# Kernel tuning notes

Measured on AMD Instinct MI355X. Metric: run time of the kernel, lower is better.

The kernel has to match this reference:

```python
import jax, jax.numpy as jnp
import numpy as np

EMIN = 1e-9
EMAX = 1.0
PENAL = 3.0
VOLFRAC = 0.4
GAMMA2 = 1.0
NME = 262144        # number of finite elements
KE = 64             # 8x8 element stiffness entries per element
NDOF = 524288       # global degrees of freedom


def setup_inputs() -> dict:
    key = jax.random.key(0)
    k1, k2, k3, k4, k5 = jax.random.split(key, 5)
    W_x = jax.random.normal(k1, (NME,), dtype=jnp.float32)
    K_sep = jax.random.normal(k2, (NME, KE), dtype=jnp.float32)
    indeces_K = jax.random.randint(k3, (2, NME * KE), 0, NDOF, dtype=jnp.int32)
    u = jax.random.normal(k4, (NDOF,), dtype=jnp.float32)
    f = jax.random.normal(k5, (NDOF,), dtype=jnp.float32)
    return {"W_x": W_x, "K_sep": K_sep, "indeces_K": indeces_K, "u": u, "f": f}


def reference(W_x, K_sep, indeces_K, u, f):
    # SIMP density from logits
    rho = jax.nn.sigmoid(W_x)                                  # [nme]
    # power-law material interpolation: Emin + rho^p (Emax - Emin)
    scale = EMIN + rho ** PENAL * (EMAX - EMIN)                # [nme]
    # scaled element stiffness values, flattened COO values
    sK = (K_sep * scale[:, None]).reshape(-1)                  # [nme*64]
    rows = indeces_K[0]
    cols = indeces_K[1]
    # sparse matvec K @ u via gather + segment-sum scatter assembly
    Ku = jax.ops.segment_sum(sK * u[cols], rows, num_segments=NDOF)  # [ndof]
    confidence_loss = jnp.linalg.norm(Ku - f)
    vofrac_loss = jax.nn.relu(rho.mean() - VOLFRAC)
    loss = vofrac_loss + GAMMA2 * confidence_loss
    return loss
```

## Files before the change

### kernel.cpp

```cpp
#include <hip/hip_runtime.h>
#include <math.h>

namespace {

constexpr int       kNME    = 262144;
constexpr int       kNDOF   = 524288;
constexpr long long kNNZ    = 16777216;
constexpr int       kNB     = 64;
constexpr int       kBShift = 13;
constexpr int       kBSpan  = 8192;
constexpr int       kEnt    = 8192;
constexpr int       kPTh   = 1024;
constexpr int       kPerTh  = 8;
constexpr int       kCtrStride = 16;
constexpr int       kScaleBlocks = kNME / 256;
constexpr int       kR      = 8;

constexpr float kEmin    = 1e-9f;
constexpr float kEmax    = 1.0f;
constexpr float kVolfrac = 0.4f;

using u32   = unsigned;
using i32x4 = __attribute__((ext_vector_type(4))) int;
using f32x4 = __attribute__((ext_vector_type(4))) float;
using u32x4 = __attribute__((ext_vector_type(4))) unsigned;

__device__ __forceinline__ u32 pack32(unsigned localrow, float v) {
    return (localrow << 19) | (__float_as_uint(v) >> 13);
}

__global__ void scale_kernel(const float* __restrict__ W_x,
                             float* __restrict__ scale,
                             float* __restrict__ acc,
                             unsigned* __restrict__ counters,
                             float* __restrict__ rho_part) {
    const int gid = blockIdx.x * blockDim.x + threadIdx.x;

    if (gid >= 1 && gid < 16) acc[gid] = 0.0f;
    const int cidx = gid - 16;
    if (cidx >= 0 && cidx < kNB * kR * kCtrStride) counters[cidx] = 0u;

    float rho = 0.0f;
    if (gid < kNME) {
        float x = W_x[gid];
        rho = 1.0f / (1.0f + __expf(-x));
        scale[gid] = kEmin + rho * rho * rho * (kEmax - kEmin);
    }
    for (int off = 32; off > 0; off >>= 1) rho += __shfl_down(rho, off, 64);
    __shared__ float partial[4];
    const int lane = threadIdx.x & 63;
    const int wid  = threadIdx.x >> 6;
    if (lane == 0) partial[wid] = rho;
    __syncthreads();
    if (threadIdx.x == 0)
        rho_part[blockIdx.x] =
            partial[0] + partial[1] + partial[2] + partial[3];
}

__global__ __launch_bounds__(kPTh, 8)
void producer_kernel(const float* __restrict__ K_sep,
                     const int*   __restrict__ rows,
                     const int*   __restrict__ cols,
                     const float* __restrict__ u,
                     const float* __restrict__ scale,
                     u32*         __restrict__ pairs,
                     unsigned*    __restrict__ counters,
                     unsigned capSub) {
    __shared__ unsigned hist[kNB], ofs[kNB], gbase[kNB];
    __shared__ u32      sorted[kEnt];

    const int tid = threadIdx.x;
    const int sub = blockIdx.x & (kR - 1);
    if (tid < kNB) hist[tid] = 0u;
    __syncthreads();

    const long long i0 =
        (long long)blockIdx.x * kEnt + (long long)tid * kPerTh;
    i32x4 r0 = __builtin_nontemporal_load((const i32x4*)(rows + i0));
    i32x4 r1 = __builtin_nontemporal_load((const i32x4*)(rows + i0) + 1);
    i32x4 c0 = __builtin_nontemporal_load((const i32x4*)(cols + i0));
    i32x4 c1 = __builtin_nontemporal_load((const i32x4*)(cols + i0) + 1);
    f32x4 k0 = __builtin_nontemporal_load((const f32x4*)(K_sep + i0));
    f32x4 k1 = __builtin_nontemporal_load((const f32x4*)(K_sep + i0) + 1);
    const float s = scale[(int)(i0 >> 6)];

    unsigned rv[kPerTh];
    float    vv[kPerTh];
#pragma unroll
    for (int j = 0; j < 4; ++j) {
        rv[j]     = (unsigned)r0[j];  vv[j]     = k0[j] * s * u[c0[j]];
        rv[j + 4] = (unsigned)r1[j];  vv[j + 4] = k1[j] * s * u[c1[j]];
    }
#pragma unroll
    for (int j = 0; j < kPerTh; ++j)
        rv[j] |= atomicAdd(&hist[rv[j] >> kBShift], 1u) << 19;
    __syncthreads();

    if (tid < kNB) {
        unsigned h = hist[tid];
        unsigned x = h;
#pragma unroll
        for (int off = 1; off < kNB; off <<= 1) {
            unsigned y = __shfl_up(x, off, 64);
            if (tid >= off) x += y;
        }
        ofs[tid]   = x - h;
        gbase[tid] = atomicAdd(&counters[(tid * kR + sub) * kCtrStride], h);
    }
    __syncthreads();

#pragma unroll
    for (int j = 0; j < kPerTh; ++j) {
        unsigned row = rv[j] & 0x7FFFFu;
        unsigned b   = row >> kBShift;
        unsigned pos = ofs[b] + (rv[j] >> 19);
        sorted[pos]  = pack32(row & (kBSpan - 1), vv[j]);
    }
    __syncthreads();

    const int wid = tid >> 6, lane = tid & 63;
    for (int b = wid; b < kNB; b += 16) {
        const unsigned s0 = ofs[b];
        const unsigned n  = hist[b];
        const unsigned g  = gbase[b];
        u32* dst = pairs + (size_t)(b * kR + sub) * capSub + g;
        for (unsigned i = lane; i < n; i += 64) {
            if (g + i < capSub) dst[i] = sorted[s0 + i];
        }
    }
}

__global__ __launch_bounds__(1024, 8)
void consumer_kernel(const u32*      __restrict__ pairs,
                     const unsigned* __restrict__ counters,
                     float*          __restrict__ partial,
                     unsigned capSub) {
    const int b   = blockIdx.x / kR;
    const int sub = blockIdx.x - b * kR;
    unsigned cnt = counters[(b * kR + sub) * kCtrStride];
    if (cnt > capSub) cnt = capSub;

    __shared__ float acc[kBSpan];
    for (int i = threadIdx.x; i < kBSpan; i += 1024) acc[i] = 0.0f;
    __syncthreads();

    const u32* p = pairs + (size_t)(b * kR + sub) * capSub;
    const unsigned aligned = cnt & ~3u;
    for (unsigned i = 4 * threadIdx.x; i < aligned; i += 4096) {
        u32x4 e = *((const u32x4*)(p + i));
#pragma unroll
        for (int j = 0; j < 4; ++j)
            atomicAdd(&acc[e[j] >> 19], __uint_as_float(e[j] << 13));
    }
    if (threadIdx.x < (cnt - aligned)) {
        u32 e = p[aligned + threadIdx.x];
        atomicAdd(&acc[e >> 19], __uint_as_float(e << 13));
    }
    __syncthreads();

    float* dst = partial + (size_t)(b * kR + sub) * kBSpan;
    for (int k = threadIdx.x; k < kBSpan; k += 1024) dst[k] = acc[k];
}

__global__ void norm_kernel(const float* __restrict__ partial,
                            const float* __restrict__ f,
                            float* __restrict__ acc,
                            const float* __restrict__ rho_part,
                            float* __restrict__ out) {
    const int b  = blockIdx.x >> 3;
    const int i0 = (blockIdx.x & 7) * 1024 + threadIdx.x * 4;
    f32x4 s = {0.0f, 0.0f, 0.0f, 0.0f};
#pragma unroll
    for (int r = 0; r < kR; ++r)
        s += *(const f32x4*)(partial + (size_t)(b * kR + r) * kBSpan + i0);
    f32x4 fv = *(const f32x4*)(f + (size_t)b * kBSpan + i0);
    f32x4 d  = s - fv;
    float a = d[0] * d[0] + d[1] * d[1] + d[2] * d[2] + d[3] * d[3];
    for (int off = 32; off > 0; off >>= 1) a += __shfl_down(a, off, 64);
    __shared__ float partial_s[4];
    const int lane = threadIdx.x & 63;
    const int wid  = threadIdx.x >> 6;
    if (lane == 0) partial_s[wid] = a;
    __syncthreads();
    if (threadIdx.x == 0) {
        atomicAdd(&acc[1],
                  partial_s[0] + partial_s[1] + partial_s[2] + partial_s[3]);
        __threadfence();
        unsigned done = atomicAdd((unsigned*)&acc[2], 1u);
        if (done == gridDim.x - 1) {
            float rs = 0.0f;
            for (int i = 0; i < kScaleBlocks; i += 4) {
                f32x4 rp = *(const f32x4*)(rho_part + i);
                rs += rp[0] + rp[1] + rp[2] + rp[3];
            }
            float ns = __hip_atomic_load(&acc[1], __ATOMIC_RELAXED,
                                         __HIP_MEMORY_SCOPE_AGENT);
            float rho_mean = rs * (1.0f / (float)kNME);
            out[0] = fmaxf(rho_mean - kVolfrac, 0.0f) + sqrtf(ns);
        }
    }
}

__global__ void scale1_kernel(const float* __restrict__ W_x,
                              float* __restrict__ scale,
                              float* __restrict__ rho_sum) {
    int i = blockIdx.x * blockDim.x + threadIdx.x;
    float rho = 0.0f;
    if (i < kNME) {
        float x = W_x[i];
        rho = 1.0f / (1.0f + __expf(-x));
        scale[i] = kEmin + rho * rho * rho * (kEmax - kEmin);
    }
    for (int off = 32; off > 0; off >>= 1) rho += __shfl_down(rho, off, 64);
    __shared__ float partial[4];
    const int lane = threadIdx.x & 63;
    const int wid  = threadIdx.x >> 6;
    if (lane == 0) partial[wid] = rho;
    __syncthreads();
    if (threadIdx.x == 0)
        atomicAdd(rho_sum, partial[0] + partial[1] + partial[2] + partial[3]);
}

__global__ void scatter_dev_kernel(const float* __restrict__ K_sep,
                                   const int*   __restrict__ rows,
                                   const int*   __restrict__ cols,
                                   const float* __restrict__ u,
                                   const float* __restrict__ scale,
                                   float* __restrict__ Ku) {
    long long i = (long long)blockIdx.x * blockDim.x + threadIdx.x;
    if (i >= kNNZ) return;
    float s = scale[(int)(i >> 6)];
    atomicAdd(&Ku[rows[i]], K_sep[i] * s * u[cols[i]]);
}

__global__ void norm1_kernel(const float* __restrict__ Ku,
                             const float* __restrict__ f,
                             float* __restrict__ norm_sum) {
    float a = 0.0f;
    for (int i = blockIdx.x * blockDim.x + threadIdx.x; i < kNDOF;
         i += gridDim.x * blockDim.x) {
        float d = Ku[i] - f[i];
        a += d * d;
    }
    for (int off = 32; off > 0; off >>= 1) a += __shfl_down(a, off, 64);
    __shared__ float partial_s[4];
    const int lane = threadIdx.x & 63;
    const int wid  = threadIdx.x >> 6;
    if (lane == 0) partial_s[wid] = a;
    __syncthreads();
    if (threadIdx.x == 0)
        atomicAdd(norm_sum,
                  partial_s[0] + partial_s[1] + partial_s[2] + partial_s[3]);
}

__global__ void finalize_kernel(const float* __restrict__ acc,
                                float* __restrict__ out) {
    if (threadIdx.x == 0 && blockIdx.x == 0) {
        float rho_mean = acc[0] * (1.0f / (float)kNME);
        float vol = fmaxf(rho_mean - kVolfrac, 0.0f);
        out[0] = vol + sqrtf(acc[1]);
    }
}

}

extern "C" void kernel_launch(void* const* d_in, const int* in_sizes, int n_in,
                              void* d_out, int out_size, void* d_ws, size_t ws_size,
                              hipStream_t stream) {
    const float* W_x   = (const float*)d_in[0];
    const float* K_sep = (const float*)d_in[1];
    const int*   idx   = (const int*)d_in[2];
    const float* u     = (const float*)d_in[3];
    const float* f     = (const float*)d_in[4];
    const int* rows = idx;
    const int* cols = idx + kNNZ;

    float* ws = (float*)d_ws;
    const size_t avail = ws_size / sizeof(float);

    const unsigned capSub = (unsigned)(kNNZ / (kNB * kR)) + 4096;
    const size_t   ctrF   = (size_t)kNB * kR * kCtrStride;
    const size_t   headF  = 16;
    const size_t   rhoF   = kScaleBlocks;
    const size_t   partF  = (size_t)kNB * kR * kBSpan;
    const size_t   need   = headF + ctrF + rhoF + partF + kNME +
                            (size_t)kNB * kR * capSub;

    if (need > avail) {
        float* Ku    = ws;
        float* scale = ws + kNDOF;
        float* acc   = ws + kNDOF + kNME;
        hipMemsetAsync(ws, 0, (size_t)(kNDOF + kNME + 16) * sizeof(float), stream);
        scale1_kernel<<<kNME / 256, 256, 0, stream>>>(W_x, scale, acc);
        scatter_dev_kernel<<<(int)(kNNZ / 256), 256, 0, stream>>>(
            K_sep, rows, cols, u, scale, Ku);
        norm1_kernel<<<2048, 256, 0, stream>>>(Ku, f, acc + 1);
        finalize_kernel<<<1, 64, 0, stream>>>(acc, (float*)d_out);
        return;
    }

    float*    acc      = ws;
    unsigned* counters = (unsigned*)(ws + headF);
    float*    rho_part = ws + headF + ctrF;
    float*    partial  = rho_part + rhoF;
    float*    scale    = partial + partF;
    u32*      pairs    = (u32*)(scale + kNME);

    scale_kernel<<<kScaleBlocks, 256, 0, stream>>>(W_x, scale, acc, counters,
                                                   rho_part);

    producer_kernel<<<(int)(kNNZ / kEnt), kPTh, 0, stream>>>(
        K_sep, rows, cols, u, scale, pairs, counters, capSub);

    consumer_kernel<<<kNB * kR, 1024, 0, stream>>>(
        pairs, counters, partial, capSub);

    norm_kernel<<<kNB * (kBSpan / 1024), 256, 0, stream>>>(
        partial, f, acc, rho_part, (float*)d_out);
}
```

Measured before the change: 242.7 us.

## Split scatter into two chunks and overlap second producer with first consumer

Splits the nonzeros into two halves with separate bucket buffers and counters. The second half's producer blocks run in the same launch as the first half's consumer blocks, interleaved 2:1 by block index, so the bandwidth-bound produce phase overlaps the LDS-atomic consume phase. A final consumer pass adds its results into the partial buffer. The cost is an extra launch, a read-modify-write of the partial buffer, and capSub slack per chunk that is tighter relative to each bucket's expected size, which raises the risk of overflow.

After: 259.5 us. 1.07x slower.

```diff
diff --git a/kernel.cpp b/kernel.cpp
--- a/kernel.cpp
+++ b/kernel.cpp
@@ -10,11 +10,14 @@
 constexpr int       kBShift = 13;
 constexpr int       kBSpan  = 8192;
 constexpr int       kEnt    = 8192;
-constexpr int       kPTh   = 1024;
+constexpr int       kPTh    = 1024;
 constexpr int       kPerTh  = 8;
 constexpr int       kCtrStride = 16;
 constexpr int       kScaleBlocks = kNME / 256;
 constexpr int       kR      = 8;
+constexpr long long kChunk  = kNNZ / 2;
+constexpr int       kPBlk   = (int)(kChunk / kEnt);
+constexpr int       kCBlk   = kNB * kR;
 
 constexpr float kEmin    = 1e-9f;
 constexpr float kEmax    = 1.0f;
@@ -29,53 +32,20 @@
     return (localrow << 19) | (__float_as_uint(v) >> 13);
 }
 
-__global__ void scale_kernel(const float* __restrict__ W_x,
-                             float* __restrict__ scale,
-                             float* __restrict__ acc,
-                             unsigned* __restrict__ counters,
-                             float* __restrict__ rho_part) {
-    const int gid = blockIdx.x * blockDim.x + threadIdx.x;
-
-    if (gid >= 1 && gid < 16) acc[gid] = 0.0f;
-    const int cidx = gid - 16;
-    if (cidx >= 0 && cidx < kNB * kR * kCtrStride) counters[cidx] = 0u;
-
-    float rho = 0.0f;
-    if (gid < kNME) {
-        float x = W_x[gid];
-        rho = 1.0f / (1.0f + __expf(-x));
-        scale[gid] = kEmin + rho * rho * rho * (kEmax - kEmin);
-    }
-    for (int off = 32; off > 0; off >>= 1) rho += __shfl_down(rho, off, 64);
-    __shared__ float partial[4];
-    const int lane = threadIdx.x & 63;
-    const int wid  = threadIdx.x >> 6;
-    if (lane == 0) partial[wid] = rho;
-    __syncthreads();
-    if (threadIdx.x == 0)
-        rho_part[blockIdx.x] =
-            partial[0] + partial[1] + partial[2] + partial[3];
-}
-
-__global__ __launch_bounds__(kPTh, 8)
-void producer_kernel(const float* __restrict__ K_sep,
-                     const int*   __restrict__ rows,
-                     const int*   __restrict__ cols,
-                     const float* __restrict__ u,
-                     const float* __restrict__ scale,
-                     u32*         __restrict__ pairs,
-                     unsigned*    __restrict__ counters,
-                     unsigned capSub) {
-    __shared__ unsigned hist[kNB], ofs[kNB], gbase[kNB];
-    __shared__ u32      sorted[kEnt];
-
+__device__ __forceinline__ void producer_body(
+    const float* __restrict__ K_sep, const int* __restrict__ rows,
+    const int* __restrict__ cols, const float* __restrict__ u,
+    const float* __restrict__ scale, u32* __restrict__ pairs,
+    unsigned* __restrict__ counters, long long chunk_base,
+    unsigned capSub, int pidx,
+    unsigned* hist, unsigned* ofs, unsigned* gbase, u32* sorted) {
     const int tid = threadIdx.x;
-    const int sub = blockIdx.x & (kR - 1);
+    const int sub = pidx & (kR - 1);
     if (tid < kNB) hist[tid] = 0u;
     __syncthreads();
 
     const long long i0 =
-        (long long)blockIdx.x * kEnt + (long long)tid * kPerTh;
+        chunk_base + (long long)pidx * kEnt + (long long)tid * kPerTh;
     i32x4 r0 = __builtin_nontemporal_load((const i32x4*)(rows + i0));
     i32x4 r1 = __builtin_nontemporal_load((const i32x4*)(rows + i0) + 1);
     i32x4 c0 = __builtin_nontemporal_load((const i32x4*)(cols + i0));
@@ -130,23 +100,21 @@
     }
 }
 
-__global__ __launch_bounds__(1024, 8)
-void consumer_kernel(const u32*      __restrict__ pairs,
-                     const unsigned* __restrict__ counters,
-                     float*          __restrict__ partial,
-                     unsigned capSub) {
-    const int b   = blockIdx.x / kR;
-    const int sub = blockIdx.x - b * kR;
+__device__ __forceinline__ void consumer_body(
+    const u32* __restrict__ pairs, const unsigned* __restrict__ counters,
+    float* __restrict__ partial, unsigned capSub, int cidx, int accum,
+    float* acc) {
+    const int b   = cidx / kR;
+    const int sub = cidx - b * kR;
     unsigned cnt = counters[(b * kR + sub) * kCtrStride];
     if (cnt > capSub) cnt = capSub;
 
-    __shared__ float acc[kBSpan];
-    for (int i = threadIdx.x; i < kBSpan; i += 1024) acc[i] = 0.0f;
+    for (int i = threadIdx.x; i < kBSpan; i += kPTh) acc[i] = 0.0f;
     __syncthreads();
 
     const u32* p = pairs + (size_t)(b * kR + sub) * capSub;
     const unsigned aligned = cnt & ~3u;
-    for (unsigned i = 4 * threadIdx.x; i < aligned; i += 4096) {
+    for (unsigned i = 4 * threadIdx.x; i < aligned; i += 4 * kPTh) {
         u32x4 e = *((const u32x4*)(p + i));
 #pragma unroll
         for (int j = 0; j < 4; ++j)
@@ -159,7 +127,79 @@
     __syncthreads();
 
     float* dst = partial + (size_t)(b * kR + sub) * kBSpan;
-    for (int k = threadIdx.x; k < kBSpan; k += 1024) dst[k] = acc[k];
+    if (accum) {
+        for (int k = threadIdx.x; k < kBSpan; k += kPTh) dst[k] += acc[k];
+    } else {
+        for (int k = threadIdx.x; k < kBSpan; k += kPTh) dst[k] = acc[k];
+    }
+}
+
+__global__ void scale_kernel(const float* __restrict__ W_x,
+                             float* __restrict__ scale,
+                             float* __restrict__ acc,
+                             unsigned* __restrict__ counters,
+                             float* __restrict__ rho_part) {
+    const int gid = blockIdx.x * blockDim.x + threadIdx.x;
+
+    if (gid >= 1 && gid < 16) acc[gid] = 0.0f;
+    const int cidx = gid - 16;
+    if (cidx >= 0 && cidx < 2 * kNB * kR * kCtrStride) counters[cidx] = 0u;
+
+    float rho = 0.0f;
+    if (gid < kNME) {
+        float x = W_x[gid];
+        rho = 1.0f / (1.0f + __expf(-x));
+        scale[gid] = kEmin + rho * rho * rho * (kEmax - kEmin);
+    }
+    for (int off = 32; off > 0; off >>= 1) rho += __shfl_down(rho, off, 64);
+    __shared__ float partial[4];
+    const int lane = threadIdx.x & 63;
+    const int wid  = threadIdx.x >> 6;
+    if (lane == 0) partial[wid] = rho;
+    __syncthreads();
+    if (threadIdx.x == 0)
+        rho_part[blockIdx.x] =
+            partial[0] + partial[1] + partial[2] + partial[3];
+}
+
+__global__ __launch_bounds__(kPTh, 8)
+void p0_kernel(const float* __restrict__ K_sep, const int* __restrict__ rows,
+               const int* __restrict__ cols, const float* __restrict__ u,
+               const float* __restrict__ scale, u32* __restrict__ pairs0,
+               unsigned* __restrict__ ctr0, unsigned capSub) {
+    __shared__ unsigned hist[kNB], ofs[kNB], gbase[kNB];
+    __shared__ __align__(16) u32 sorted[kEnt];
+    producer_body(K_sep, rows, cols, u, scale, pairs0, ctr0, 0LL, capSub,
+                  blockIdx.x, hist, ofs, gbase, sorted);
+}
+
+__global__ __launch_bounds__(kPTh, 8)
+void p1c0_kernel(const float* __restrict__ K_sep, const int* __restrict__ rows,
+                 const int* __restrict__ cols, const float* __restrict__ u,
+                 const float* __restrict__ scale,
+                 u32* __restrict__ pairs0, u32* __restrict__ pairs1,
+                 unsigned* __restrict__ ctr0, unsigned* __restrict__ ctr1,
+                 float* __restrict__ partial, unsigned capSub) {
+    __shared__ unsigned hist[kNB], ofs[kNB], gbase[kNB];
+    __shared__ __align__(16) u32 sorted[kEnt];
+
+    const int i = blockIdx.x;
+    if ((i % 3) != 2) {
+        const int pidx = (i / 3) * 2 + (i % 3);
+        producer_body(K_sep, rows, cols, u, scale, pairs1, ctr1, kChunk,
+                      capSub, pidx, hist, ofs, gbase, sorted);
+    } else {
+        const int cidx = i / 3;
+        consumer_body(pairs0, ctr0, partial, capSub, cidx, 0,
+                      (float*)sorted);
+    }
+}
+
+__global__ __launch_bounds__(kPTh, 8)
+void c1_kernel(const u32* __restrict__ pairs1, const unsigned* __restrict__ ctr1,
+               float* __restrict__ partial, unsigned capSub) {
+    __shared__ __align__(16) float acc[kBSpan];
+    consumer_body(pairs1, ctr1, partial, capSub, blockIdx.x, 1, acc);
 }
 
 __global__ void norm_kernel(const float* __restrict__ partial,
@@ -278,13 +318,14 @@
     float* ws = (float*)d_ws;
     const size_t avail = ws_size / sizeof(float);
 
-    const unsigned capSub = (unsigned)(kNNZ / (kNB * kR)) + 4096;
+    const unsigned capSub = (unsigned)(kChunk / (kNB * kR)) + 2048;
     const size_t   ctrF   = (size_t)kNB * kR * kCtrStride;
     const size_t   headF  = 16;
     const size_t   rhoF   = kScaleBlocks;
     const size_t   partF  = (size_t)kNB * kR * kBSpan;
-    const size_t   need   = headF + ctrF + rhoF + partF + kNME +
-                            (size_t)kNB * kR * capSub;
+    const size_t   pairF  = (size_t)kNB * kR * capSub;
+    const size_t   need   = headF + 2 * ctrF + rhoF + partF + kNME +
+                            2 * pairF;
 
     if (need > avail) {
         float* Ku    = ws;
@@ -300,20 +341,25 @@
     }
 
     float*    acc      = ws;
-    unsigned* counters = (unsigned*)(ws + headF);
-    float*    rho_part = ws + headF + ctrF;
+    unsigned* ctr0     = (unsigned*)(ws + headF);
+    unsigned* ctr1     = ctr0 + ctrF;
+    float*    rho_part = ws + headF + 2 * ctrF;
     float*    partial  = rho_part + rhoF;
     float*    scale    = partial + partF;
-    u32*      pairs    = (u32*)(scale + kNME);
-
-    scale_kernel<<<kScaleBlocks, 256, 0, stream>>>(W_x, scale, acc, counters,
+    u32*      pairs0   = (u32*)(scale + kNME);
+    u32*      pairs1   = pairs0 + pairF;
+
+    scale_kernel<<<kScaleBlocks, 256, 0, stream>>>(W_x, scale, acc, ctr0,
                                                    rho_part);
 
-    producer_kernel<<<(int)(kNNZ / kEnt), kPTh, 0, stream>>>(
-        K_sep, rows, cols, u, scale, pairs, counters, capSub);
-
-    consumer_kernel<<<kNB * kR, 1024, 0, stream>>>(
-        pairs, counters, partial, capSub);
+    p0_kernel<<<kPBlk, kPTh, 0, stream>>>(K_sep, rows, cols, u, scale,
+                                          pairs0, ctr0, capSub);
+
+    p1c0_kernel<<<kPBlk + kCBlk, kPTh, 0, stream>>>(
+        K_sep, rows, cols, u, scale, pairs0, pairs1, ctr0, ctr1, partial,
+        capSub);
+
+    c1_kernel<<<kCBlk, kPTh, 0, stream>>>(pairs1, ctr1, partial, capSub);
 
     norm_kernel<<<kNB * (kBSpan / 1024), 256, 0, stream>>>(
         partial, f, acc, rho_part, (float*)d_out);
```

## Use 512 finer row buckets and fuse consumer accumulation with norm reduction

Applied to the files above, without the earlier changes.

Rows are now split into 512 buckets of 1024 rows instead of 64 buckets with 8 sub-slots. Each consumer block accumulates one full bucket in a 1 KB shared tile and computes the squared residual against f directly, so the partial-sum buffer and the separate norm kernel go away. Packed values keep 22 mantissa-truncated bits instead of 19, which improves precision. The costs are a two-level prefix scan in the producer, scattered writes split into 16-lane groups across more buckets, and more contention on the shared global counters.

New measurement: 263.9 us. 8.7% more time.

```diff
diff --git a/kernel.cpp b/kernel.cpp
--- a/kernel.cpp
+++ b/kernel.cpp
@@ -6,15 +6,14 @@
 constexpr int       kNME    = 262144;
 constexpr int       kNDOF   = 524288;
 constexpr long long kNNZ    = 16777216;
-constexpr int       kNB     = 64;
-constexpr int       kBShift = 13;
-constexpr int       kBSpan  = 8192;
+constexpr int       kNBk    = 512;
+constexpr int       kBSh    = 10;
+constexpr int       kBSp    = 1024;
 constexpr int       kEnt    = 8192;
-constexpr int       kPTh   = 1024;
+constexpr int       kPTh    = 1024;
 constexpr int       kPerTh  = 8;
 constexpr int       kCtrStride = 16;
 constexpr int       kScaleBlocks = kNME / 256;
-constexpr int       kR      = 8;
 
 constexpr float kEmin    = 1e-9f;
 constexpr float kEmax    = 1.0f;
@@ -26,7 +25,7 @@
 using u32x4 = __attribute__((ext_vector_type(4))) unsigned;
 
 __device__ __forceinline__ u32 pack32(unsigned localrow, float v) {
-    return (localrow << 19) | (__float_as_uint(v) >> 13);
+    return (localrow << 22) | (__float_as_uint(v) >> 10);
 }
 
 __global__ void scale_kernel(const float* __restrict__ W_x,
@@ -38,7 +37,7 @@
 
     if (gid >= 1 && gid < 16) acc[gid] = 0.0f;
     const int cidx = gid - 16;
-    if (cidx >= 0 && cidx < kNB * kR * kCtrStride) counters[cidx] = 0u;
+    if (cidx >= 0 && cidx < kNBk * kCtrStride) counters[cidx] = 0u;
 
     float rho = 0.0f;
     if (gid < kNME) {
@@ -66,12 +65,12 @@
                      u32*         __restrict__ pairs,
                      unsigned*    __restrict__ counters,
                      unsigned capSub) {
-    __shared__ unsigned hist[kNB], ofs[kNB], gbase[kNB];
+    __shared__ unsigned hist[kNBk], ofs[kNBk], gbase[kNBk];
+    __shared__ unsigned wtot[8], woff[8];
     __shared__ u32      sorted[kEnt];
 
     const int tid = threadIdx.x;
-    const int sub = blockIdx.x & (kR - 1);
-    if (tid < kNB) hist[tid] = 0u;
+    if (tid < kNBk) hist[tid] = 0u;
     __syncthreads();
 
     const long long i0 =
@@ -93,98 +92,105 @@
     }
 #pragma unroll
     for (int j = 0; j < kPerTh; ++j)
-        rv[j] |= atomicAdd(&hist[rv[j] >> kBShift], 1u) << 19;
-    __syncthreads();
-
-    if (tid < kNB) {
-        unsigned h = hist[tid];
-        unsigned x = h;
-#pragma unroll
-        for (int off = 1; off < kNB; off <<= 1) {
+        rv[j] |= atomicAdd(&hist[rv[j] >> kBSh], 1u) << 19;
+    __syncthreads();
+
+    unsigned h = 0, x = 0;
+    if (tid < kNBk) {
+        h = hist[tid];
+        x = h;
+#pragma unroll
+        for (int off = 1; off < 64; off <<= 1) {
             unsigned y = __shfl_up(x, off, 64);
-            if (tid >= off) x += y;
+            if ((tid & 63) >= off) x += y;
         }
-        ofs[tid]   = x - h;
-        gbase[tid] = atomicAdd(&counters[(tid * kR + sub) * kCtrStride], h);
+        if ((tid & 63) == 63) wtot[tid >> 6] = x;
+    }
+    __syncthreads();
+    if (tid < 8) {
+        unsigned t  = wtot[tid];
+        unsigned xx = t;
+#pragma unroll
+        for (int off = 1; off < 8; off <<= 1) {
+            unsigned y = __shfl_up(xx, off, 64);
+            if (tid >= off) xx += y;
+        }
+        woff[tid] = xx - t;
+    }
+    __syncthreads();
+    if (tid < kNBk) {
+        ofs[tid]   = woff[tid >> 6] + x - h;
+        gbase[tid] = atomicAdd(&counters[tid * kCtrStride], h);
     }
     __syncthreads();
 
 #pragma unroll
     for (int j = 0; j < kPerTh; ++j) {
         unsigned row = rv[j] & 0x7FFFFu;
-        unsigned b   = row >> kBShift;
+        unsigned b   = row >> kBSh;
         unsigned pos = ofs[b] + (rv[j] >> 19);
-        sorted[pos]  = pack32(row & (kBSpan - 1), vv[j]);
+        sorted[pos]  = pack32(row & (kBSp - 1), vv[j]);
     }
     __syncthreads();
 
     const int wid = tid >> 6, lane = tid & 63;
-    for (int b = wid; b < kNB; b += 16) {
+    const int qw  = lane >> 4, ql = lane & 15;
+    for (int r4 = wid * 4; r4 < kNBk; r4 += 64) {
+        const int b = r4 + qw;
         const unsigned s0 = ofs[b];
         const unsigned n  = hist[b];
         const unsigned g  = gbase[b];
-        u32* dst = pairs + (size_t)(b * kR + sub) * capSub + g;
-        for (unsigned i = lane; i < n; i += 64) {
+        u32* dst = pairs + (size_t)b * capSub + g;
+        for (unsigned i = ql; i < n; i += 16) {
             if (g + i < capSub) dst[i] = sorted[s0 + i];
         }
     }
 }
 
 __global__ __launch_bounds__(1024, 8)
-void consumer_kernel(const u32*      __restrict__ pairs,
-                     const unsigned* __restrict__ counters,
-                     float*          __restrict__ partial,
-                     unsigned capSub) {
-    const int b   = blockIdx.x / kR;
-    const int sub = blockIdx.x - b * kR;
-    unsigned cnt = counters[(b * kR + sub) * kCtrStride];
+void consumer_norm_kernel(const u32*      __restrict__ pairs,
+                          const unsigned* __restrict__ counters,
+                          const float*    __restrict__ f,
+                          float*          __restrict__ acc,
+                          const float*    __restrict__ rho_part,
+                          float*          __restrict__ out,
+                          unsigned capSub) {
+    const int b = blockIdx.x;
+    __shared__ float tile[kBSp];
+    __shared__ float partial_s[16];
+    if (threadIdx.x < kBSp) tile[threadIdx.x] = 0.0f;
+    __syncthreads();
+
+    unsigned cnt = counters[b * kCtrStride];
     if (cnt > capSub) cnt = capSub;
-
-    __shared__ float acc[kBSpan];
-    for (int i = threadIdx.x; i < kBSpan; i += 1024) acc[i] = 0.0f;
-    __syncthreads();
-
-    const u32* p = pairs + (size_t)(b * kR + sub) * capSub;
+    const u32* p = pairs + (size_t)b * capSub;
     const unsigned aligned = cnt & ~3u;
     for (unsigned i = 4 * threadIdx.x; i < aligned; i += 4096) {
         u32x4 e = *((const u32x4*)(p + i));
 #pragma unroll
         for (int j = 0; j < 4; ++j)
-            atomicAdd(&acc[e[j] >> 19], __uint_as_float(e[j] << 13));
+            atomicAdd(&tile[e[j] >> 22], __uint_as_float(e[j] << 10));
     }
     if (threadIdx.x < (cnt - aligned)) {
         u32 e = p[aligned + threadIdx.x];
-        atomicAdd(&acc[e >> 19], __uint_as_float(e << 13));
-    }
-    __syncthreads();
-
-    float* dst = partial + (size_t)(b * kR + sub) * kBSpan;
-    for (int k = threadIdx.x; k < kBSpan; k += 1024) dst[k] = acc[k];
-}
-
-__global__ void norm_kernel(const float* __restrict__ partial,
-                            const float* __restrict__ f,
-                            float* __restrict__ acc,
-                            const float* __restrict__ rho_part,
-                            float* __restrict__ out) {
-    const int b  = blockIdx.x >> 3;
-    const int i0 = (blockIdx.x & 7) * 1024 + threadIdx.x * 4;
-    f32x4 s = {0.0f, 0.0f, 0.0f, 0.0f};
-#pragma unroll
-    for (int r = 0; r < kR; ++r)
-        s += *(const f32x4*)(partial + (size_t)(b * kR + r) * kBSpan + i0);
-    f32x4 fv = *(const f32x4*)(f + (size_t)b * kBSpan + i0);
-    f32x4 d  = s - fv;
-    float a = d[0] * d[0] + d[1] * d[1] + d[2] * d[2] + d[3] * d[3];
+        atomicAdd(&tile[e >> 22], __uint_as_float(e << 10));
+    }
+    __syncthreads();
+
+    float a = 0.0f;
+    {
+        float d = tile[threadIdx.x] - f[(size_t)b * kBSp + threadIdx.x];
+        a = d * d;
+    }
     for (int off = 32; off > 0; off >>= 1) a += __shfl_down(a, off, 64);
-    __shared__ float partial_s[4];
-    const int lane = threadIdx.x & 63;
-    const int wid  = threadIdx.x >> 6;
+    const int lane = threadIdx.x & 63, wid = threadIdx.x >> 6;
     if (lane == 0) partial_s[wid] = a;
     __syncthreads();
     if (threadIdx.x == 0) {
-        atomicAdd(&acc[1],
-                  partial_s[0] + partial_s[1] + partial_s[2] + partial_s[3]);
+        float t = 0.0f;
+#pragma unroll
+        for (int w = 0; w < 16; ++w) t += partial_s[w];
+        atomicAdd(&acc[1], t);
         __threadfence();
         unsigned done = atomicAdd((unsigned*)&acc[2], 1u);
         if (done == gridDim.x - 1) {
@@ -278,13 +284,12 @@
     float* ws = (float*)d_ws;
     const size_t avail = ws_size / sizeof(float);
 
-    const unsigned capSub = (unsigned)(kNNZ / (kNB * kR)) + 4096;
-    const size_t   ctrF   = (size_t)kNB * kR * kCtrStride;
+    const unsigned capSub = (unsigned)(kNNZ / kNBk) + 2048;
+    const size_t   ctrF   = (size_t)kNBk * kCtrStride;
     const size_t   headF  = 16;
     const size_t   rhoF   = kScaleBlocks;
-    const size_t   partF  = (size_t)kNB * kR * kBSpan;
-    const size_t   need   = headF + ctrF + rhoF + partF + kNME +
-                            (size_t)kNB * kR * capSub;
+    const size_t   need   = headF + ctrF + rhoF + kNME +
+                            (size_t)kNBk * capSub;
 
     if (need > avail) {
         float* Ku    = ws;
@@ -302,8 +307,7 @@
     float*    acc      = ws;
     unsigned* counters = (unsigned*)(ws + headF);
     float*    rho_part = ws + headF + ctrF;
-    float*    partial  = rho_part + rhoF;
-    float*    scale    = partial + partF;
+    float*    scale    = rho_part + rhoF;
     u32*      pairs    = (u32*)(scale + kNME);
 
     scale_kernel<<<kScaleBlocks, 256, 0, stream>>>(W_x, scale, acc, counters,
@@ -312,9 +316,6 @@
     producer_kernel<<<(int)(kNNZ / kEnt), kPTh, 0, stream>>>(
         K_sep, rows, cols, u, scale, pairs, counters, capSub);
 
-    consumer_kernel<<<kNB * kR, 1024, 0, stream>>>(
-        pairs, counters, partial, capSub);
-
-    norm_kernel<<<kNB * (kBSpan / 1024), 256, 0, stream>>>(
-        partial, f, acc, rho_part, (float*)d_out);
-}
+    consumer_norm_kernel<<<kNBk, 1024, 0, stream>>>(
+        pairs, counters, f, acc, rho_part, (float*)d_out, capSub);
+}
```
